# Kernel tuning notes

Measured on AMD Instinct MI355X. Metric: run time of the kernel, lower is better.

## Reference

```python
import jax, jax.numpy as jnp
import numpy as np

DIM = 512
NUM_HEADS = 8
HEAD_DIM = DIM // NUM_HEADS        # 64
L_HEADS = 4                        # int(8 * 0.5)
H_HEADS = NUM_HEADS - L_HEADS      # 4
L_DIM = L_HEADS * HEAD_DIM         # 256
H_DIM = H_HEADS * HEAD_DIM         # 256
WS = 2                             # window_size
SCALE = HEAD_DIM ** -0.5
SEQ_LEN = 1024


def setup_inputs() -> dict:
    key = jax.random.key(0)
    ks = jax.random.split(key, 13)
    B, N, C = 16, 1024, DIM
    def w(k, shape, fan_in):
        return (jax.random.normal(k, shape, jnp.float32) / np.sqrt(fan_in)).astype(jnp.float32)
    return {
        "x": jax.random.normal(ks[0], (B, N, C), jnp.float32),
        "pos_emb": jax.random.normal(ks[1], (1, SEQ_LEN, C), jnp.float32) * 0.02,
        "l_q_w": w(ks[2], (C, L_DIM), C),
        "l_kv_w": w(ks[3], (C, 2 * L_DIM), C),
        "l_proj_w": w(ks[4], (L_DIM, L_DIM), L_DIM),
        "l_proj_b": jax.random.normal(ks[5], (L_DIM,), jnp.float32) * 0.01,
        "h_qkv_w": w(ks[6], (C, 3 * H_DIM), C),
        "h_proj_w": w(ks[7], (H_DIM, H_DIM), H_DIM),
        "h_proj_b": jax.random.normal(ks[8], (H_DIM,), jnp.float32) * 0.01,
        "in_proj_w": w(ks[9], (C, 3 * C), C),
        "in_proj_b": jax.random.normal(ks[10], (3 * C,), jnp.float32) * 0.01,
        "out_proj_w": w(ks[11], (C, C), C),
        "out_proj_b": jax.random.normal(ks[12], (C,), jnp.float32) * 0.01,
        "H": 32,
        "W": 32,
    }


def _hifi(xg, h_qkv_w, h_proj_w, h_proj_b, H, W):
    B, _, _, C = xg.shape
    hg, wg = H // WS, W // WS
    G, T = hg * wg, WS * WS
    # [B, hg, WS, wg, WS, C] -> [B, G, T, C] (window partition)
    xw = xg.reshape(B, hg, WS, wg, WS, C).transpose(0, 1, 3, 2, 4, 5).reshape(B, G, T, C)
    qkv = (xw @ h_qkv_w).reshape(B, G, T, 3, H_HEADS, HEAD_DIM)
    q = qkv[:, :, :, 0].transpose(0, 1, 3, 2, 4)  # [B,G,h,T,d]
    k = qkv[:, :, :, 1].transpose(0, 1, 3, 2, 4)
    v = qkv[:, :, :, 2].transpose(0, 1, 3, 2, 4)
    attn = jax.nn.softmax(jnp.einsum("bghtd,bghsd->bghts", q, k) * SCALE, axis=-1)
    o = jnp.einsum("bghts,bghsd->bghtd", attn, v)
    # window un-partition: [B,G,h,T,d] -> [B,H,W,h_dim]
    o = o.transpose(0, 1, 3, 2, 4).reshape(B, hg, wg, WS, WS, H_DIM)
    o = o.transpose(0, 1, 3, 2, 4, 5).reshape(B, H, W, H_DIM)
    return o @ h_proj_w + h_proj_b


def _lofi(xg, l_q_w, l_kv_w, l_proj_w, l_proj_b, H, W):
    B, _, _, C = xg.shape
    N = H * W
    q = (xg @ l_q_w).reshape(B, N, L_HEADS, HEAD_DIM)
    kv = (xg @ l_kv_w).reshape(B, N, 2, L_HEADS, HEAD_DIM)
    k, v = kv[:, :, 0], kv[:, :, 1]
    attn = jax.nn.softmax(jnp.einsum("bnhd,bmhd->bhnm", q, k) * SCALE, axis=-1)
    o = jnp.einsum("bhnm,bmhd->bnhd", attn, v).reshape(B, H, W, L_DIM)
    return o @ l_proj_w + l_proj_b


def _mha(y, in_proj_w, in_proj_b, out_proj_w, out_proj_b):
    B, N, C = y.shape
    qkv = y @ in_proj_w + in_proj_b
    q, k, v = jnp.split(qkv, 3, axis=-1)
    q = q.reshape(B, N, NUM_HEADS, HEAD_DIM)
    k = k.reshape(B, N, NUM_HEADS, HEAD_DIM)
    v = v.reshape(B, N, NUM_HEADS, HEAD_DIM)
    attn = jax.nn.softmax(jnp.einsum("bnhd,bmhd->bhnm", q, k) * SCALE, axis=-1)
    o = jnp.einsum("bhnm,bmhd->bnhd", attn, v).reshape(B, N, C)
    return o @ out_proj_w + out_proj_b


def reference(x, pos_emb, l_q_w, l_kv_w, l_proj_w, l_proj_b,
              h_qkv_w, h_proj_w, h_proj_b,
              in_proj_w, in_proj_b, out_proj_w, out_proj_b, H, W):
    B, N, C = x.shape
    x = x + pos_emb[:, :N, :]
    xg = x.reshape(B, H, W, C)
    hifi_out = _hifi(xg, h_qkv_w, h_proj_w, h_proj_b, H, W)
    lofi_out = _lofi(xg, l_q_w, l_kv_w, l_proj_w, l_proj_b, H, W)
    y = jnp.concatenate([hifi_out, lofi_out], axis=-1).reshape(B, N, C)
    return _mha(y, in_proj_w, in_proj_b, out_proj_w, out_proj_b)
```

## Files before the change

kernel.cpp:

```cpp
#include <hip/hip_runtime.h>

typedef unsigned short ushort_t;
typedef short bf16x8 __attribute__((ext_vector_type(8)));
typedef float f32x4 __attribute__((ext_vector_type(4)));

#define DEV __device__ __forceinline__

DEV ushort_t f2bf(float f) {
  return (ushort_t)((__float_as_uint(f) + 0x8000u) >> 16);
}
DEV unsigned pk_bf16(float lo, float hi) {
  unsigned a = __float_as_uint(lo) + 0x8000u;
  unsigned b = __float_as_uint(hi) + 0x8000u;
  return __builtin_amdgcn_perm(b, a, 0x07060302);
}
DEV float bf2f(ushort_t h) {
  union { unsigned int u; float f; } v; v.u = ((unsigned int)h) << 16;
  return v.f;
}
DEV f32x4 mfma16(bf16x8 a, bf16x8 b, f32x4 c) {
  return __builtin_amdgcn_mfma_f32_16x16x32_bf16(a, b, c, 0, 0, 0);
}
typedef __attribute__((address_space(3))) void lds_void;
typedef const __attribute__((address_space(1))) void glb_void;
DEV void gl_lds16(const void* g, void* l) {
  __builtin_amdgcn_global_load_lds((glb_void*)g, (lds_void*)l, 16, 0, 0);
}

__global__ __launch_bounds__(256)
void gemm_bt(const ushort_t* __restrict__ A, int lda,
             const ushort_t* __restrict__ BT,
             const float* __restrict__ bias,
             ushort_t* __restrict__ Cb, float* __restrict__ Cf,
             int ldc, int coff, int K, float scv, int sc_lo, int sc_hi)
{
  __shared__ __align__(16) ushort_t As[128 * 32];
  __shared__ __align__(16) ushort_t Bs[128 * 32];
  const int tid  = threadIdx.x;
  const int wave = tid >> 6, lane = tid & 63;
  const int quad = lane >> 4, r16 = lane & 15;
  const int m0 = blockIdx.x * 128, n0 = blockIdx.y * 128;
  const int wm = (wave >> 1) * 64, wn = (wave & 1) * 64;

  f32x4 acc[4][4];
#pragma unroll
  for (int i = 0; i < 4; ++i)
#pragma unroll
    for (int j = 0; j < 4; ++j) acc[i][j] = (f32x4){0.f, 0.f, 0.f, 0.f};

  for (int kc = 0; kc < K; kc += 32) {
#pragma unroll
    for (int p = 0; p < 4; ++p) {
      int wp = p * 4 + wave;
      int lc = ((wp & 7) << 6) + lane;
      int row = lc >> 2, e8 = (lc & 3) * 8;
      if (wp < 8) gl_lds16(&A[(size_t)(m0 + row) * lda + kc + e8], &As[lc * 8]);
      else        gl_lds16(&BT[(size_t)(n0 + row) * K  + kc + e8], &Bs[lc * 8]);
    }
    __syncthreads();
    bf16x8 af[4], bfr[4];
#pragma unroll
    for (int i = 0; i < 4; ++i) {
      af[i]  = *(const bf16x8*)&As[(wm + i * 16 + r16) * 32 + quad * 8];
      bfr[i] = *(const bf16x8*)&Bs[(wn + i * 16 + r16) * 32 + quad * 8];
    }
#pragma unroll
    for (int mi = 0; mi < 4; ++mi)
#pragma unroll
      for (int ni = 0; ni < 4; ++ni)
        acc[mi][ni] = mfma16(af[mi], bfr[ni], acc[mi][ni]);
    __syncthreads();
  }

#pragma unroll
  for (int mi = 0; mi < 4; ++mi) {
#pragma unroll
    for (int ni = 0; ni < 4; ++ni) {
      int col = n0 + wn + ni * 16 + r16;
      float bv = bias ? bias[col] : 0.f;
      float s = (col >= sc_lo && col < sc_hi) ? scv : 1.0f;
#pragma unroll
      for (int r = 0; r < 4; ++r) {
        int row = m0 + wm + mi * 16 + quad * 4 + r;
        float v = (acc[mi][ni][r] + bv) * s;
        if (Cf) Cf[(size_t)row * ldc + coff + col] = v;
        else    Cb[(size_t)row * ldc + coff + col] = f2bf(v);
      }
    }
  }
}

__global__ __launch_bounds__(256)
void flash_attn7(const ushort_t* __restrict__ Q, int qs, int q_ch,
                 const ushort_t* __restrict__ Kg, int ks, int k_ch,
                 const ushort_t* __restrict__ vT,
                 ushort_t* __restrict__ O, int os, int o_ch,
                 int N)
{
  __shared__ __align__(16) ushort_t Ks[2][2][64 * 32];
  __shared__ __align__(16) ushort_t Vs[2][2][64 * 32];

  const int b = blockIdx.z, h = blockIdx.y, H = gridDim.y;
  const int tid = threadIdx.x, wave = tid >> 6, lane = tid & 63;
  const int quad = lane >> 4, c16 = lane & 15;
  const int q0 = blockIdx.x * 128 + wave * 32;

  bf16x8 qf[2][2];
#pragma unroll
  for (int qt = 0; qt < 2; ++qt) {
    const ushort_t* qp = Q + ((size_t)b * N + q0 + qt * 16 + c16) * qs + q_ch + h * 64;
    qf[qt][0] = *(const bf16x8*)&qp[quad * 8];
    qf[qt][1] = *(const bf16x8*)&qp[32 + quad * 8];
  }
  const ushort_t* kbase = Kg + ((size_t)b * N) * ks + k_ch + h * 64;
  const ushort_t* vbase = vT + ((size_t)(b * H + h) * 64) * N;

  f32x4 oacc[2][4];
#pragma unroll
  for (int qt = 0; qt < 2; ++qt)
#pragma unroll
    for (int dt = 0; dt < 4; ++dt) oacc[qt][dt] = (f32x4){0.f, 0.f, 0.f, 0.f};
  float l_acc[2] = {0.f, 0.f};

  const int laneA = (2 * (quad & 1)) * 16 + c16;
  const int laneB = laneA + 16;

  auto stage = [&](int s0, int buf) {
#pragma unroll
    for (int p = 0; p < 4; ++p) {
      int wp = p * 4 + wave;
      int lc = ((wp & 3) << 6) + lane;
      int row = lc >> 2, e8 = (lc & 3) * 8;
      if (wp < 4)       gl_lds16(kbase + (size_t)(s0 + row) * ks + e8,      &Ks[buf][0][lc * 8]);
      else if (wp < 8)  gl_lds16(kbase + (size_t)(s0 + row) * ks + 32 + e8, &Ks[buf][1][lc * 8]);
      else if (wp < 12) gl_lds16(vbase + (size_t)row * N + s0 + e8,         &Vs[buf][0][lc * 8]);
      else              gl_lds16(vbase + (size_t)row * N + s0 + 32 + e8,    &Vs[buf][1][lc * 8]);
    }
  };

  stage(0, 0);
  const int NT = N >> 6;
  for (int it = 0; it < NT; ++it) {
    const int cur = it & 1;
    __syncthreads();
    if (it + 1 < NT) stage((it + 1) << 6, cur ^ 1);

    f32x4 st[4][2];
#pragma unroll
    for (int si = 0; si < 4; ++si) {
      bf16x8 kf0 = *(const bf16x8*)&Ks[cur][0][(si * 16 + c16) * 32 + quad * 8];
      bf16x8 kf1 = *(const bf16x8*)&Ks[cur][1][(si * 16 + c16) * 32 + quad * 8];
#pragma unroll
      for (int qt = 0; qt < 2; ++qt) {
        f32x4 z = (f32x4){0.f, 0.f, 0.f, 0.f};
        z = mfma16(kf0, qf[qt][0], z);
        z = mfma16(kf1, qf[qt][1], z);
        st[si][qt] = z;
      }
    }

#pragma unroll
    for (int qt = 0; qt < 2; ++qt) {
      float tsum = 0.f;
      unsigned pks[4][2];
#pragma unroll
      for (int si = 0; si < 4; ++si) {
        float p0 = __expf(st[si][qt][0]);
        float p1 = __expf(st[si][qt][1]);
        float p2 = __expf(st[si][qt][2]);
        float p3 = __expf(st[si][qt][3]);
        tsum += (p0 + p1) + (p2 + p3);
        pks[si][0] = pk_bf16(p0, p1);
        pks[si][1] = pk_bf16(p2, p3);
      }
      l_acc[qt] += tsum;

      union U8 { bf16x8 f; unsigned u[4]; } pf0, pf1;
      const bool hiq = quad >= 2;
#pragma unroll
      for (int i = 0; i < 4; ++i) {
        int src = (i < 2) ? laneA : laneB;
        unsigned a0 = __shfl(pks[0][i & 1], src);
        unsigned a1 = __shfl(pks[1][i & 1], src);
        unsigned a2 = __shfl(pks[2][i & 1], src);
        unsigned a3 = __shfl(pks[3][i & 1], src);
        pf0.u[i] = hiq ? a1 : a0;
        pf1.u[i] = hiq ? a3 : a2;
      }

#pragma unroll
      for (int dt = 0; dt < 4; ++dt) {
        bf16x8 vf0 = *(const bf16x8*)&Vs[cur][0][(dt * 16 + c16) * 32 + quad * 8];
        bf16x8 vf1 = *(const bf16x8*)&Vs[cur][1][(dt * 16 + c16) * 32 + quad * 8];
        oacc[qt][dt] = mfma16(vf0, pf0.f, oacc[qt][dt]);
        oacc[qt][dt] = mfma16(vf1, pf1.f, oacc[qt][dt]);
      }
    }
  }

#pragma unroll
  for (int qt = 0; qt < 2; ++qt) {
    float l = l_acc[qt];
    l += __shfl_xor(l, 16);
    l += __shfl_xor(l, 32);
    float inv = 1.f / l;
    ushort_t* op = O + ((size_t)b * N + q0 + qt * 16 + c16) * os + o_ch + h * 64;
#pragma unroll
    for (int dt = 0; dt < 4; ++dt) {
      uint2 pkv;
      pkv.x = pk_bf16(oacc[qt][dt][0] * inv, oacc[qt][dt][1] * inv);
      pkv.y = pk_bf16(oacc[qt][dt][2] * inv, oacc[qt][dt][3] * inv);
      *(uint2*)&op[dt * 16 + quad * 4] = pkv;
    }
  }
}

__global__ __launch_bounds__(256)
void transpose_v(const ushort_t* __restrict__ in, int ld, int ch,
                 ushort_t* __restrict__ out, int N, int H)
{
  __shared__ __align__(16) ushort_t T[64][72];
  const int s0 = blockIdx.x * 64, h = blockIdx.y, b = blockIdx.z;
  const int tid = threadIdx.x;
#pragma unroll
  for (int p = 0; p < 2; ++p) {
    int c = p * 256 + tid;
    int sr = c >> 3, d0 = (c & 7) * 8;
    *(uint4*)&T[sr][d0] =
        *(const uint4*)&in[((size_t)b * N + s0 + sr) * ld + ch + h * 64 + d0];
  }
  __syncthreads();
  const int d = tid >> 2, sp = (tid & 3) * 16;
  union { uint4 v; ushort_t u[8]; } A, B;
#pragma unroll
  for (int j = 0; j < 8; ++j) { A.u[j] = T[sp + j][d]; B.u[j] = T[sp + 8 + j][d]; }
  ushort_t* op = out + ((size_t)(b * H + h) * 64 + d) * N + s0 + sp;
  *(uint4*)&op[0] = A.v;
  *(uint4*)&op[8] = B.v;
}

__global__ __launch_bounds__(256)
void hifi_win(const ushort_t* __restrict__ qkv, int ld, ushort_t* __restrict__ out)
{
  const int bg = blockIdx.x;
  const int b = bg >> 8, g = bg & 255;
  const int head = threadIdx.x >> 6, lane = threadIdx.x & 63;
  const int gh = g >> 4, gw = g & 15;

  int n[4];
  float q[4], k[4], v[4];
#pragma unroll
  for (int t = 0; t < 4; ++t) {
    n[t] = (gh * 2 + (t >> 1)) * 32 + gw * 2 + (t & 1);
    size_t base = ((size_t)b * 1024 + n[t]) * ld + head * 64 + lane;
    q[t] = bf2f(qkv[base]);
    k[t] = bf2f(qkv[base + 256]);
    v[t] = bf2f(qkv[base + 512]);
  }
  float sc[4][4];
#pragma unroll
  for (int t = 0; t < 4; ++t)
#pragma unroll
    for (int s = 0; s < 4; ++s) {
      float p = q[t] * k[s];
#pragma unroll
      for (int off = 32; off >= 1; off >>= 1) p += __shfl_xor(p, off);
      sc[t][s] = p * 0.125f;
    }
#pragma unroll
  for (int t = 0; t < 4; ++t) {
    float m = fmaxf(fmaxf(sc[t][0], sc[t][1]), fmaxf(sc[t][2], sc[t][3]));
    float p0 = __expf(sc[t][0] - m), p1 = __expf(sc[t][1] - m);
    float p2 = __expf(sc[t][2] - m), p3 = __expf(sc[t][3] - m);
    float sum = p0 + p1 + p2 + p3;
    float o = (p0 * v[0] + p1 * v[1] + p2 * v[2] + p3 * v[3]) / sum;
    out[((size_t)b * 1024 + n[t]) * 512 + head * 64 + lane] = f2bf(o);
  }
}

struct WEnt { const float* W; ushort_t* WT; int K; int N; };
struct WArgs { WEnt e[7]; };

__global__ __launch_bounds__(256)
void w_prep(WArgs a)
{
  WEnt w = a.e[blockIdx.z];
  if ((int)blockIdx.x >= (w.K >> 6) || (int)blockIdx.y >= (w.N >> 6)) return;
  __shared__ float T[64][65];
  const int k0 = blockIdx.x * 64, n0 = blockIdx.y * 64;
  const int tid = threadIdx.x;
#pragma unroll
  for (int p = 0; p < 4; ++p) {
    int c = p * 256 + tid;
    int kr = c >> 4, f4 = (c & 15) * 4;
    float4 v = *(const float4*)&w.W[(size_t)(k0 + kr) * w.N + n0 + f4];
    T[f4 + 0][kr] = v.x; T[f4 + 1][kr] = v.y;
    T[f4 + 2][kr] = v.z; T[f4 + 3][kr] = v.w;
  }
  __syncthreads();
  const int nl = tid >> 2, kp = (tid & 3) * 16;
  union { uint4 v; ushort_t u[8]; } A, B;
#pragma unroll
  for (int j = 0; j < 8; ++j) {
    A.u[j] = f2bf(T[nl][kp + j]);
    B.u[j] = f2bf(T[nl][kp + 8 + j]);
  }
  ushort_t* op = w.WT + (size_t)(n0 + nl) * w.K + k0 + kp;
  *(uint4*)&op[0] = A.v;
  *(uint4*)&op[8] = B.v;
}

__global__ void add_pos(const float* __restrict__ x, const float* __restrict__ pos,
                        ushort_t* __restrict__ xpe)
{
  int idx = blockIdx.x * 256 + threadIdx.x;
  int e = idx * 4;
  float4 xv = *(const float4*)&x[e];
  float4 pv = *(const float4*)&pos[e & (512 * 1024 - 1)];
  uint2 pk;
  pk.x = pk_bf16(xv.x + pv.x, xv.y + pv.y);
  pk.y = pk_bf16(xv.z + pv.z, xv.w + pv.w);
  *(uint2*)&xpe[e] = pk;
}

extern "C" void kernel_launch(void* const* d_in, const int* in_sizes, int n_in,
                              void* d_out, int out_size, void* d_ws, size_t ws_size,
                              hipStream_t stream)
{
  const float* x         = (const float*)d_in[0];
  const float* pos       = (const float*)d_in[1];
  const float* l_q_w     = (const float*)d_in[2];
  const float* l_kv_w    = (const float*)d_in[3];
  const float* l_proj_w  = (const float*)d_in[4];
  const float* l_proj_b  = (const float*)d_in[5];
  const float* h_qkv_w   = (const float*)d_in[6];
  const float* h_proj_w  = (const float*)d_in[7];
  const float* h_proj_b  = (const float*)d_in[8];
  const float* in_proj_w = (const float*)d_in[9];
  const float* in_proj_b = (const float*)d_in[10];
  const float* out_proj_w= (const float*)d_in[11];
  const float* out_proj_b= (const float*)d_in[12];
  float* out = (float*)d_out;

  const float QSCALE = 0.125f;

  char* ws = (char*)d_ws;
  ushort_t* xpe = (ushort_t*)(ws);
  ushort_t* y   = (ushort_t*)(ws + (size_t)16777216);
  ushort_t* F   = (ushort_t*)(ws + (size_t)33554432);
  ushort_t* rB  = (ushort_t*)(ws + (size_t)83886080);
  ushort_t* wb  = (ushort_t*)(ws + (size_t)100663296);

  ushort_t* F_T      = wb;
  ushort_t* h_projT  = wb + 786432;
  ushort_t* l_projT  = wb + 851968;
  ushort_t* in_projT = wb + 917504;
  ushort_t* out_projT= wb + 1703936;

  const int M = 16384;
  ushort_t* vT_lo = xpe;
  ushort_t* vT_m  = rB;

  WArgs wa;
  wa.e[0] = {h_qkv_w,   F_T,                 512, 768};
  wa.e[1] = {l_q_w,     F_T + 768 * 512,     512, 256};
  wa.e[2] = {l_kv_w,    F_T + 1024 * 512,    512, 512};
  wa.e[3] = {h_proj_w,  h_projT,             256, 256};
  wa.e[4] = {l_proj_w,  l_projT,             256, 256};
  wa.e[5] = {in_proj_w, in_projT,            512, 1536};
  wa.e[6] = {out_proj_w,out_projT,           512, 512};
  w_prep<<<dim3(8, 24, 7), dim3(256), 0, stream>>>(wa);

  add_pos<<<dim3(8192), dim3(256), 0, stream>>>(x, pos, xpe);

  gemm_bt<<<dim3(M / 128, 12), dim3(256), 0, stream>>>(
      xpe, 512, F_T, nullptr, F, nullptr, 1536, 0, 512, QSCALE, 768, 1024);
  hifi_win<<<dim3(4096), dim3(256), 0, stream>>>(F, 1536, rB);
  transpose_v<<<dim3(16, 4, 16), dim3(256), 0, stream>>>(
      F, 1536, 1280, vT_lo, 1024, 4);
  flash_attn7<<<dim3(8, 4, 16), dim3(256), 0, stream>>>(
      F, 1536, 768, F, 1536, 1024, vT_lo, rB, 512, 256, 1024);
  gemm_bt<<<dim3(M / 128, 2), dim3(256), 0, stream>>>(
      rB, 512, h_projT, h_proj_b, y, nullptr, 512, 0, 256, 1.0f, 0, 0);
  gemm_bt<<<dim3(M / 128, 2), dim3(256), 0, stream>>>(
      rB + 256, 512, l_projT, l_proj_b, y, nullptr, 512, 256, 256, 1.0f, 0, 0);
  gemm_bt<<<dim3(M / 128, 12), dim3(256), 0, stream>>>(
      y, 512, in_projT, in_proj_b, F, nullptr, 1536, 0, 512, QSCALE, 0, 512);
  transpose_v<<<dim3(16, 8, 16), dim3(256), 0, stream>>>(
      F, 1536, 1024, vT_m, 1024, 8);
  flash_attn7<<<dim3(8, 8, 16), dim3(256), 0, stream>>>(
      F, 1536, 0, F, 1536, 512, vT_m, xpe, 512, 0, 1024);
  gemm_bt<<<dim3(M / 128, 4), dim3(256), 0, stream>>>(
      xpe, 512, out_projT, out_proj_b, nullptr, out, 512, 0, 512, 1.0f, 0, 0);
}
```

Baseline: 371.0 us.

## Swizzle flash-attention LDS layout, remap workgroups, use exp2 with folded log2e

Merges the split 32-column K/V LDS tiles into one 64-column tile with an XOR swizzle on both the global-to-LDS stores and the fragment reads, aiming to reduce LDS bank conflicts. It also remaps block indices so consecutive workgroups spread across XCDs while the 8 query blocks of a (batch, head) pair are grouped, replaces __expf with native exp2 by folding log2(e) into the Q scale, and hoists V fragment loads so each is reused across both query tiles. The block remapping hardcodes 8 query blocks and assumes H is 8 or 4, so other shapes would compute wrong indices.

Result: faster. 363.3 us (-2.1%).

```diff
diff --git a/kernel.cpp b/kernel.cpp
--- a/kernel.cpp
+++ b/kernel.cpp
@@ -97,13 +97,21 @@
                  ushort_t* __restrict__ O, int os, int o_ch,
                  int N)
 {
-  __shared__ __align__(16) ushort_t Ks[2][2][64 * 32];
-  __shared__ __align__(16) ushort_t Vs[2][2][64 * 32];
-
-  const int b = blockIdx.z, h = blockIdx.y, H = gridDim.y;
+  __shared__ __align__(16) ushort_t Ks[2][64 * 64];
+  __shared__ __align__(16) ushort_t Vs[2][64 * 64];
+
+  const int H = gridDim.y;
   const int tid = threadIdx.x, wave = tid >> 6, lane = tid & 63;
   const int quad = lane >> 4, c16 = lane & 15;
-  const int q0 = blockIdx.x * 128 + wave * 32;
+
+  const int nwg = gridDim.x * H * gridDim.z;
+  const int lin = blockIdx.x + gridDim.x * (blockIdx.y + H * blockIdx.z);
+  const int logical = (lin & 7) * (nwg >> 3) + (lin >> 3);
+  const int qb = logical & 7;
+  const int t8 = logical >> 3;
+  const int b = (H == 8) ? (t8 >> 3) : (t8 >> 2);
+  const int h = t8 - b * H;
+  const int q0 = qb * 128 + wave * 32;
 
   bf16x8 qf[2][2];
 #pragma unroll
@@ -125,16 +133,18 @@
   const int laneA = (2 * (quad & 1)) * 16 + c16;
   const int laneB = laneA + 16;
 
+  const int eo0 = (quad ^ (c16 & 7)) * 8;
+  const int eo1 = eo0 ^ 32;
+
   auto stage = [&](int s0, int buf) {
 #pragma unroll
     for (int p = 0; p < 4; ++p) {
       int wp = p * 4 + wave;
-      int lc = ((wp & 3) << 6) + lane;
-      int row = lc >> 2, e8 = (lc & 3) * 8;
-      if (wp < 4)       gl_lds16(kbase + (size_t)(s0 + row) * ks + e8,      &Ks[buf][0][lc * 8]);
-      else if (wp < 8)  gl_lds16(kbase + (size_t)(s0 + row) * ks + 32 + e8, &Ks[buf][1][lc * 8]);
-      else if (wp < 12) gl_lds16(vbase + (size_t)row * N + s0 + e8,         &Vs[buf][0][lc * 8]);
-      else              gl_lds16(vbase + (size_t)row * N + s0 + 32 + e8,    &Vs[buf][1][lc * 8]);
+      int lc = ((wp & 7) << 6) + lane;
+      int row = lc >> 3, c = lc & 7;
+      int e8 = ((c ^ (row & 7)) * 8);
+      if (wp < 8) gl_lds16(kbase + (size_t)(s0 + row) * ks + e8, &Ks[buf][lc * 8]);
+      else        gl_lds16(vbase + (size_t)row * N + s0 + e8,    &Vs[buf][lc * 8]);
     }
   };
 
@@ -148,8 +158,9 @@
     f32x4 st[4][2];
 #pragma unroll
     for (int si = 0; si < 4; ++si) {
-      bf16x8 kf0 = *(const bf16x8*)&Ks[cur][0][(si * 16 + c16) * 32 + quad * 8];
-      bf16x8 kf1 = *(const bf16x8*)&Ks[cur][1][(si * 16 + c16) * 32 + quad * 8];
+      const ushort_t* kr = &Ks[cur][(si * 16 + c16) * 64];
+      bf16x8 kf0 = *(const bf16x8*)&kr[eo0];
+      bf16x8 kf1 = *(const bf16x8*)&kr[eo1];
 #pragma unroll
       for (int qt = 0; qt < 2; ++qt) {
         f32x4 z = (f32x4){0.f, 0.f, 0.f, 0.f};
@@ -159,16 +170,17 @@
       }
     }
 
+    bf16x8 pA[2], pB[2];
 #pragma unroll
     for (int qt = 0; qt < 2; ++qt) {
       float tsum = 0.f;
       unsigned pks[4][2];
 #pragma unroll
       for (int si = 0; si < 4; ++si) {
-        float p0 = __expf(st[si][qt][0]);
-        float p1 = __expf(st[si][qt][1]);
-        float p2 = __expf(st[si][qt][2]);
-        float p3 = __expf(st[si][qt][3]);
+        float p0 = __builtin_amdgcn_exp2f(st[si][qt][0]);
+        float p1 = __builtin_amdgcn_exp2f(st[si][qt][1]);
+        float p2 = __builtin_amdgcn_exp2f(st[si][qt][2]);
+        float p3 = __builtin_amdgcn_exp2f(st[si][qt][3]);
         tsum += (p0 + p1) + (p2 + p3);
         pks[si][0] = pk_bf16(p0, p1);
         pks[si][1] = pk_bf16(p2, p3);
@@ -187,13 +199,19 @@
         pf0.u[i] = hiq ? a1 : a0;
         pf1.u[i] = hiq ? a3 : a2;
       }
-
-#pragma unroll
-      for (int dt = 0; dt < 4; ++dt) {
-        bf16x8 vf0 = *(const bf16x8*)&Vs[cur][0][(dt * 16 + c16) * 32 + quad * 8];
-        bf16x8 vf1 = *(const bf16x8*)&Vs[cur][1][(dt * 16 + c16) * 32 + quad * 8];
-        oacc[qt][dt] = mfma16(vf0, pf0.f, oacc[qt][dt]);
-        oacc[qt][dt] = mfma16(vf1, pf1.f, oacc[qt][dt]);
+      pA[qt] = pf0.f;
+      pB[qt] = pf1.f;
+    }
+
+#pragma unroll
+    for (int dt = 0; dt < 4; ++dt) {
+      const ushort_t* vr = &Vs[cur][(dt * 16 + c16) * 64];
+      bf16x8 vf0 = *(const bf16x8*)&vr[eo0];
+      bf16x8 vf1 = *(const bf16x8*)&vr[eo1];
+#pragma unroll
+      for (int qt = 0; qt < 2; ++qt) {
+        oacc[qt][dt] = mfma16(vf0, pA[qt], oacc[qt][dt]);
+        oacc[qt][dt] = mfma16(vf1, pB[qt], oacc[qt][dt]);
       }
     }
   }
@@ -342,7 +360,7 @@
   const float* out_proj_b= (const float*)d_in[12];
   float* out = (float*)d_out;
 
-  const float QSCALE = 0.125f;
+  const float QSCALE = 0.125f * 1.44269504f;
 
   char* ws = (char*)d_ws;
   ushort_t* xpe = (ushort_t*)(ws);
```
